# Optimization experiments

Hardware: AMD Instinct MI355X
Metric: run time of the kernel (lower is better)

The kernel has to match this reference:

```python
import jax, jax.numpy as jnp
import numpy as np

DIM = 512        # model dim
MOE_DIM = 256    # expert hidden dim
E = 64           # n_routed experts
G = 8            # n_routed_group
TOPK_G = 4       # n_topk_group
K = 8            # n_experts_per_tok
SCALE = 2.5      # routed_scale
CAP = 1024


def setup_inputs() -> dict:
    key = jax.random.key(0)
    ks = jax.random.split(key, 6)
    x = jax.random.normal(ks[0], (4, 512, DIM), jnp.float32)
    gate_w = jax.random.normal(ks[1], (E, DIM), jnp.float32) / np.sqrt(DIM).astype(np.float32)
    gate_b = jax.random.normal(ks[2], (E,), jnp.float32) * 0.01
    w1 = jax.random.normal(ks[3], (E, DIM, MOE_DIM), jnp.float32) / np.sqrt(DIM).astype(np.float32)
    w3 = jax.random.normal(ks[4], (E, DIM, MOE_DIM), jnp.float32) / np.sqrt(DIM).astype(np.float32)
    w2 = jax.random.normal(ks[5], (E, MOE_DIM, DIM), jnp.float32) / np.sqrt(MOE_DIM).astype(np.float32)
    return {"x": x, "gate_w": gate_w, "gate_b": gate_b, "w1": w1, "w3": w3, "w2": w2}


def _gate(x2, gate_w, gate_b):
    # x2: [T, DIM] -> (weights [T,K], indices [T,K])
    T = x2.shape[0]
    scores = jax.nn.sigmoid(x2 @ gate_w.T)                      # [T, E]
    s = (scores + gate_b).reshape(T, G, E // G)                  # grouped scores
    group_scores = jax.lax.top_k(s, 2)[0].sum(-1)                # [T, G] sum of top-2 per group
    top_groups = jax.lax.top_k(group_scores, TOPK_G)[1]          # [T, TOPK_G]
    gmask = jnp.zeros((T, G), bool).at[jnp.arange(T)[:, None], top_groups].set(True)
    s = jnp.where(gmask[..., None], s, -jnp.inf).reshape(T, E)
    idx = jax.lax.top_k(s, K)[1]                                 # [T, K]
    w = jnp.take_along_axis(scores, idx, axis=1)                 # original (pre-bias) scores
    w = w / w.sum(-1, keepdims=True) * SCALE
    return w, idx


def _moe_forward(x, gate_w, gate_b, w1, w3, w2):
    shape = x.shape
    x2 = x.reshape(-1, DIM)                                      # [T, DIM]
    T = x2.shape[0]
    w, idx = _gate(x2, gate_w, gate_b)
    flat_e = idx.reshape(-1)                                     # [T*K]
    # position of each (token, slot) within its expert's buffer, in order
    oh = (flat_e[:, None] == jnp.arange(E)[None, :]).astype(jnp.int32)  # [T*K, E]
    pos = (jnp.cumsum(oh, axis=0) * oh).sum(-1) - 1              # [T*K]
    x_rep = jnp.repeat(x2, K, axis=0)                            # [T*K, DIM]
    # dispatch into per-expert buffers [E, CAP, DIM]
    xb = jnp.zeros((E, CAP, DIM), x2.dtype).at[flat_e, pos].set(x_rep, mode='drop')
    h = jax.nn.silu(jnp.einsum('ecd,edm->ecm', xb, w1)) * jnp.einsum('ecd,edm->ecm', xb, w3)
    yb = jnp.einsum('ecm,emd->ecd', h, w2)                       # [E, CAP, DIM]
    # combine: gather back and weight
    y = yb.at[flat_e, pos].get(mode='fill', fill_value=0.0) * w.reshape(-1)[:, None]
    return y.reshape(T, K, DIM).sum(1).reshape(shape)


def reference(x, gate_w, gate_b, w1, w3, w2):
    return _moe_forward(x, gate_w, gate_b, w1, w3, w2)
```

## Files before the change

### kernel.cpp

```cpp
#include <hip/hip_runtime.h>

#define T_TOK 2048
#define DIM   512
#define MOE   256
#define NE    64
#define NG    8
#define TOPKG 4
#define TOPK  8
#define CAP   1024
#define MOE_SCALE 2.5f

typedef float f32x4 __attribute__((ext_vector_type(4)));
typedef short s16x8 __attribute__((ext_vector_type(8)));

__device__ __forceinline__ unsigned short f2bf(float f) {
    unsigned u = __builtin_bit_cast(unsigned, f);
    unsigned r = (u + 0x7fffu + ((u >> 16) & 1u)) >> 16;
    return (unsigned short)r;
}
__device__ __forceinline__ unsigned pk2(float lo, float hi) {
    return (unsigned)f2bf(lo) | ((unsigned)f2bf(hi) << 16);
}

__global__ __launch_bounds__(256) void gwt_k(const float* __restrict__ gw,
                                             float* __restrict__ gwT)
{
    int idx = blockIdx.x * 256 + threadIdx.x;
    int e = idx >> 9, k = idx & 511;
    gwT[(size_t)(k >> 2) * 256 + e * 4 + (k & 3)] = gw[idx];
}

__global__ __launch_bounds__(256) void gate_fused_k(const float* __restrict__ x,
                                                    const float* __restrict__ gwT,
                                                    const float* __restrict__ gb,
                                                    int* __restrict__ counts,
                                                    int* __restrict__ etok,
                                                    float* __restrict__ wt_of,
                                                    short* __restrict__ xb)
{
    __shared__ float xs[4][512];
    int w = threadIdx.x >> 6, lane = threadIdx.x & 63;
    int t = blockIdx.x * 4 + w;

    {
        const float4* xr = (const float4*)(x + (size_t)t * DIM);
        float4 v0 = xr[lane * 2], v1 = xr[lane * 2 + 1];
        *(float4*)&xs[w][lane * 8]     = v0;
        *(float4*)&xs[w][lane * 8 + 4] = v1;
        short o[8];
        o[0] = (short)f2bf(v0.x); o[1] = (short)f2bf(v0.y);
        o[2] = (short)f2bf(v0.z); o[3] = (short)f2bf(v0.w);
        o[4] = (short)f2bf(v1.x); o[5] = (short)f2bf(v1.y);
        o[6] = (short)f2bf(v1.z); o[7] = (short)f2bf(v1.w);
        *(s16x8*)(xb + (size_t)t * DIM + lane * 8) = *(const s16x8*)o;
    }
    __syncthreads();

    const float4* gt = (const float4*)gwT;
    float a0 = 0.f, a1 = 0.f, a2 = 0.f, a3 = 0.f;
#pragma unroll 4
    for (int k4 = 0; k4 < 128; k4 += 4) {
        float4 g0 = gt[(k4 + 0) * 64 + lane];
        float4 g1 = gt[(k4 + 1) * 64 + lane];
        float4 g2 = gt[(k4 + 2) * 64 + lane];
        float4 g3 = gt[(k4 + 3) * 64 + lane];
        float4 x0 = *(const float4*)&xs[w][(k4 + 0) * 4];
        float4 x1 = *(const float4*)&xs[w][(k4 + 1) * 4];
        float4 x2 = *(const float4*)&xs[w][(k4 + 2) * 4];
        float4 x3 = *(const float4*)&xs[w][(k4 + 3) * 4];
        a0 += g0.x * x0.x + g0.y * x0.y + g0.z * x0.z + g0.w * x0.w;
        a1 += g1.x * x1.x + g1.y * x1.y + g1.z * x1.z + g1.w * x1.w;
        a2 += g2.x * x2.x + g2.y * x2.y + g2.z * x2.z + g2.w * x2.w;
        a3 += g3.x * x3.x + g3.y * x3.y + g3.z * x3.z + g3.w * x3.w;
    }
    float acc = (a0 + a1) + (a2 + a3);
    float sc = 1.f / (1.f + __expf(-acc));
    float s  = sc + gb[lane];

    float m1 = s, m2 = -1e30f;
#pragma unroll
    for (int d = 1; d < 8; d <<= 1) {
        float o1 = __shfl_xor(m1, d);
        float o2 = __shfl_xor(m2, d);
        float n1 = fmaxf(m1, o1);
        float n2 = fmaxf(fminf(m1, o1), fmaxf(m2, o2));
        m1 = n1; m2 = n2;
    }
    float gv = m1 + m2;

    bool gkeep = false;
#pragma unroll
    for (int it = 0; it < TOPKG; ++it) {
        float m = gv;
#pragma unroll
        for (int d = 1; d < 64; d <<= 1) m = fmaxf(m, __shfl_xor(m, d));
        unsigned long long mask = __ballot(gv == m);
        int ldr = __ffsll(mask) - 1;
        if ((lane >> 3) == (ldr >> 3)) { gkeep = true; gv = -2e30f; }
    }
    float sv = gkeep ? s : -1e30f;

    float wsum = 0.f;
    int my_e = 0; float my_w = 0.f;
#pragma unroll
    for (int k = 0; k < TOPK; ++k) {
        float m = sv;
#pragma unroll
        for (int d = 1; d < 64; d <<= 1) m = fmaxf(m, __shfl_xor(m, d));
        unsigned long long mask = __ballot(sv == m);
        int l = __ffsll(mask) - 1;
        float wk = __shfl(sc, l);
        wsum += wk;
        if (lane == k) { my_e = l; my_w = wk; }
        if (lane == l) sv = -2e30f;
    }
    float scale = MOE_SCALE / wsum;
    if (lane < TOPK) {
        int p = atomicAdd(&counts[my_e], 1);
        int rid = t * TOPK + lane;
        bool ok = (p < CAP);
        if (ok) etok[my_e * CAP + p] = rid;
        wt_of[rid] = ok ? my_w * scale : 0.f;
    }
}

__global__ __launch_bounds__(64) void scan_k(const int* __restrict__ counts,
                                             int* __restrict__ tbase)
{
    int lane = threadIdx.x;
    int ne = min(counts[lane], CAP);
    int nt = (ne + 31) >> 5;
    int v = nt;
#pragma unroll
    for (int d = 1; d < 64; d <<= 1) {
        int o = __shfl_up(v, d);
        if (lane >= d) v += o;
    }
    tbase[lane] = v - nt;
}

__global__ __launch_bounds__(256, 3) void gemm1_k(const short* __restrict__ xb,
                                                  const float* __restrict__ w1,
                                                  const float* __restrict__ w3,
                                                  const int* __restrict__ counts,
                                                  const int* __restrict__ etok,
                                                  const int* __restrict__ tbase,
                                                  short* __restrict__ hgf)
{
    __shared__ short Bl[2][16][64][8];
    __shared__ short Ct[4][2][16][24];

    int e  = blockIdx.x & 63, cg = blockIdx.x >> 6;
    int n0 = cg * 16;
    int tid = threadIdx.x;
    int w = tid >> 6, lane = tid & 63;
    int q = lane >> 4, m16 = lane & 15;

    const float* W1e = w1 + (size_t)e * DIM * MOE + n0;
    const float* W3e = w3 + (size_t)e * DIM * MOE + n0;
#pragma unroll 4
    for (int it = 0; it < 8; ++it) {
        int idx = it * 256 + tid;
        int mat = idx >> 10;
        int rem = idx & 1023;
        int r2  = rem >> 2;
        int cq  = (rem & 3) * 4;
        int k   = r2 * 2;
        int kt = k >> 5, qf = (k >> 3) & 3, j0 = k & 7;
        const float* p = (mat ? W3e : W1e) + (size_t)k * MOE + cq;
        float4 lo = *(const float4*)p;
        float4 hi = *(const float4*)(p + MOE);
        unsigned* b = (unsigned*)&Bl[mat][kt][qf * 16 + cq][j0];
        b[0]  = pk2(lo.x, hi.x);
        b[4]  = pk2(lo.y, hi.y);
        b[8]  = pk2(lo.z, hi.z);
        b[12] = pk2(lo.w, hi.w);
    }
    __syncthreads();

    int ne = min(counts[e], CAP);
    int nt = (ne + 31) >> 5;
    int G0 = tbase[e];
    const int* el = etok + e * CAP;

    for (int T = w; T < nt; T += 4) {
        int row0 = T * 32 + m16, row1 = T * 32 + 16 + m16;
        int tok0 = el[row0 < ne ? row0 : ne - 1] >> 3;
        int tok1 = el[row1 < ne ? row1 : ne - 1] >> 3;
        const short* A0 = xb + (size_t)tok0 * DIM + q * 8;
        const short* A1 = xb + (size_t)tok1 * DIM + q * 8;

        f32x4 acc[2][2];
#pragma unroll
        for (int j = 0; j < 2; ++j)
#pragma unroll
            for (int m = 0; m < 2; ++m) acc[j][m] = (f32x4)0.f;

        s16x8 a0 = *(const s16x8*)(A0);
        s16x8 a1 = *(const s16x8*)(A1);
#pragma unroll
        for (int kt = 0; kt < 16; ++kt) {
            s16x8 a0n, a1n;
            if (kt < 15) {
                a0n = *(const s16x8*)(A0 + (kt + 1) * 32);
                a1n = *(const s16x8*)(A1 + (kt + 1) * 32);
            }
            s16x8 b1 = *(const s16x8*)&Bl[0][kt][lane][0];
            s16x8 b3 = *(const s16x8*)&Bl[1][kt][lane][0];
            acc[0][0] = __builtin_amdgcn_mfma_f32_16x16x32_bf16(a0, b1, acc[0][0], 0, 0, 0);
            acc[1][0] = __builtin_amdgcn_mfma_f32_16x16x32_bf16(a1, b1, acc[1][0], 0, 0, 0);
            acc[0][1] = __builtin_amdgcn_mfma_f32_16x16x32_bf16(a0, b3, acc[0][1], 0, 0, 0);
            acc[1][1] = __builtin_amdgcn_mfma_f32_16x16x32_bf16(a1, b3, acc[1][1], 0, 0, 0);
            a0 = a0n; a1 = a1n;
        }

#pragma unroll
        for (int sub = 0; sub < 2; ++sub)
#pragma unroll
            for (int r = 0; r < 4; ++r) {
                float g = acc[sub][0][r];
                float u = acc[sub][1][r];
                float hv = g / (1.f + __expf(-g)) * u;
                Ct[w][sub][q * 4 + r][m16] = (short)f2bf(hv);
            }
        int sub = q >> 1;
        s16x8 hv8 = *(const s16x8*)&Ct[w][sub][m16][(q & 1) * 8];
        size_t slot = ((size_t)(G0 + T) * 8 + (cg >> 1)) * 2 + sub;
        *(s16x8*)(hgf + slot * 512 + ((cg & 1) * 2 + (q & 1)) * 128 + m16 * 8) = hv8;
    }
}

__global__ __launch_bounds__(256, 3) void gemm2_k(const short* __restrict__ hgf,
                                                  const float* __restrict__ w2,
                                                  const int* __restrict__ counts,
                                                  const int* __restrict__ etok,
                                                  const int* __restrict__ tbase,
                                                  short* __restrict__ ybuf)
{
    __shared__ short Bl[2][8][64][8];

    int e  = blockIdx.x & 63, cg = blockIdx.x >> 6;
    int n0 = cg * 32;
    int tid = threadIdx.x;
    int w = tid >> 6, lane = tid & 63;
    int q = lane >> 4, m16 = lane & 15;

    const float* W2e = w2 + (size_t)e * MOE * DIM + n0;
#pragma unroll 4
    for (int it = 0; it < 4; ++it) {
        int idx = it * 256 + tid;
        int r2  = idx >> 3;
        int cq  = (idx & 7) * 4;
        int k   = r2 * 2;
        int kt2 = k >> 5, qf = (k >> 3) & 3, j0 = k & 7;
        int s = cq >> 4, c15 = cq & 15;
        const float* p = W2e + (size_t)k * DIM + cq;
        float4 lo = *(const float4*)p;
        float4 hi = *(const float4*)(p + DIM);
        unsigned* b = (unsigned*)&Bl[s][kt2][qf * 16 + c15][j0];
        b[0]  = pk2(lo.x, hi.x);
        b[4]  = pk2(lo.y, hi.y);
        b[8]  = pk2(lo.z, hi.z);
        b[12] = pk2(lo.w, hi.w);
    }
    __syncthreads();

    int ne = min(counts[e], CAP);
    int nt = (ne + 31) >> 5;
    int G0 = tbase[e];
    const int* el = etok + e * CAP;

    for (int T = w; T < nt; T += 4) {
        const short* A = hgf + (size_t)(G0 + T) * 8192 + lane * 8;

        f32x4 acc[2][2];
#pragma unroll
        for (int j = 0; j < 2; ++j)
#pragma unroll
            for (int m = 0; m < 2; ++m) acc[j][m] = (f32x4)0.f;

        s16x8 a0 = *(const s16x8*)(A);
        s16x8 a1 = *(const s16x8*)(A + 512);
#pragma unroll
        for (int kt = 0; kt < 8; ++kt) {
            s16x8 a0n, a1n;
            if (kt < 7) {
                a0n = *(const s16x8*)(A + (size_t)((kt + 1) * 2 + 0) * 512);
                a1n = *(const s16x8*)(A + (size_t)((kt + 1) * 2 + 1) * 512);
            }
            s16x8 b0 = *(const s16x8*)&Bl[0][kt][lane][0];
            s16x8 b1 = *(const s16x8*)&Bl[1][kt][lane][0];
            acc[0][0] = __builtin_amdgcn_mfma_f32_16x16x32_bf16(a0, b0, acc[0][0], 0, 0, 0);
            acc[1][0] = __builtin_amdgcn_mfma_f32_16x16x32_bf16(a1, b0, acc[1][0], 0, 0, 0);
            acc[0][1] = __builtin_amdgcn_mfma_f32_16x16x32_bf16(a0, b1, acc[0][1], 0, 0, 0);
            acc[1][1] = __builtin_amdgcn_mfma_f32_16x16x32_bf16(a1, b1, acc[1][1], 0, 0, 0);
            a0 = a0n; a1 = a1n;
        }

#pragma unroll
        for (int sub = 0; sub < 2; ++sub)
#pragma unroll
            for (int s = 0; s < 2; ++s)
#pragma unroll
                for (int r = 0; r < 4; ++r) {
                    int row = T * 32 + sub * 16 + q * 4 + r;
                    if (row < ne)
                        ybuf[(size_t)el[row] * DIM + n0 + s * 16 + m16] =
                            (short)f2bf(acc[sub][s][r]);
                }
    }
}

__global__ __launch_bounds__(256) void combine_k(const short* __restrict__ ybuf,
                                                 const float* __restrict__ wt_of,
                                                 float* __restrict__ out)
{
    int t = blockIdx.x;
    int tid = threadIdx.x;
    const int* yb = (const int*)ybuf;
    float sx = 0.f, sy = 0.f;
#pragma unroll
    for (int k = 0; k < TOPK; ++k) {
        float wk = wt_of[t * TOPK + k];
        int v = yb[(size_t)(t * TOPK + k) * (DIM / 2) + tid];
        float lo = __builtin_bit_cast(float, (unsigned)v << 16);
        float hi = __builtin_bit_cast(float, (unsigned)v & 0xffff0000u);
        sx += wk * lo;
        sy += wk * hi;
    }
    float2 o = {sx, sy};
    ((float2*)out)[(size_t)t * (DIM / 2) + tid] = o;
}

extern "C" void kernel_launch(void* const* d_in, const int* in_sizes, int n_in,
                              void* d_out, int out_size, void* d_ws, size_t ws_size,
                              hipStream_t stream)
{
    const float* x  = (const float*)d_in[0];
    const float* gw = (const float*)d_in[1];
    const float* gb = (const float*)d_in[2];
    const float* w1 = (const float*)d_in[3];
    const float* w3 = (const float*)d_in[4];
    const float* w2 = (const float*)d_in[5];

    char* ws = (char*)d_ws;
    short* xb    = (short*)(ws);
    short* hgf   = (short*)(ws + 2097152);
    short* ybuf  = (short*)(ws + 11534336);
    float* gwT   = (float*)(ws + 28311552);
    int*   etok  = (int*)  (ws + 28442624);
    float* wt_of = (float*)(ws + 28704768);
    int*   counts= (int*)  (ws + 28770304);
    int*   tbase = (int*)  (ws + 28770560);

    hipMemsetAsync(counts, 0, NE * 4, stream);

    gwt_k<<<128, 256, 0, stream>>>(gw, gwT);
    gate_fused_k<<<T_TOK / 4, 256, 0, stream>>>(x, gwT, gb, counts, etok, wt_of, xb);
    scan_k<<<1, 64, 0, stream>>>(counts, tbase);
    gemm1_k<<<NE * 16, 256, 0, stream>>>(xb, w1, w3, counts, etok, tbase, hgf);
    gemm2_k<<<NE * 16, 256, 0, stream>>>(hgf, w2, counts, etok, tbase, ybuf);
    combine_k<<<T_TOK, 256, 0, stream>>>(ybuf, wt_of, (float*)d_out);
}
```

Before: 248.8 us.

## Widen expert GEMM column tiles, deepen A prefetch, split gate dot over waves

Each expert GEMM block now covers twice as many output columns, using 32 for gemm1 and 64 for gemm2, with half as many blocks. This reuses each gathered A fragment across more MFMAs and halves how often activations are re-read per expert. A loads are prefetched four k-steps ahead, the next tile's token indices are prefetched, and weight loads use nontemporal hints. The gate kernel splits the K dimension across waves so each gwT load is shared by four tokens, then reduces the partial sums through shared memory. The trade-off is higher register and LDS use, with launch bounds lowered to two blocks, and fewer blocks to spread the load across CUs.

```diff
diff --git a/kernel.cpp b/kernel.cpp
--- a/kernel.cpp
+++ b/kernel.cpp
@@ -39,6 +39,7 @@
                                                     short* __restrict__ xb)
 {
     __shared__ float xs[4][512];
+    __shared__ float ps[4][4][64];
     int w = threadIdx.x >> 6, lane = threadIdx.x & 63;
     int t = blockIdx.x * 4 + w;
 
@@ -56,24 +57,26 @@
     }
     __syncthreads();
 
-    const float4* gt = (const float4*)gwT;
+    const f32x4* gt = (const f32x4*)gwT;
     float a0 = 0.f, a1 = 0.f, a2 = 0.f, a3 = 0.f;
-#pragma unroll 4
-    for (int k4 = 0; k4 < 128; k4 += 4) {
-        float4 g0 = gt[(k4 + 0) * 64 + lane];
-        float4 g1 = gt[(k4 + 1) * 64 + lane];
-        float4 g2 = gt[(k4 + 2) * 64 + lane];
-        float4 g3 = gt[(k4 + 3) * 64 + lane];
-        float4 x0 = *(const float4*)&xs[w][(k4 + 0) * 4];
-        float4 x1 = *(const float4*)&xs[w][(k4 + 1) * 4];
-        float4 x2 = *(const float4*)&xs[w][(k4 + 2) * 4];
-        float4 x3 = *(const float4*)&xs[w][(k4 + 3) * 4];
-        a0 += g0.x * x0.x + g0.y * x0.y + g0.z * x0.z + g0.w * x0.w;
-        a1 += g1.x * x1.x + g1.y * x1.y + g1.z * x1.z + g1.w * x1.w;
-        a2 += g2.x * x2.x + g2.y * x2.y + g2.z * x2.z + g2.w * x2.w;
-        a3 += g3.x * x3.x + g3.y * x3.y + g3.z * x3.z + g3.w * x3.w;
-    }
-    float acc = (a0 + a1) + (a2 + a3);
+    int kb = w * 32;
+#pragma unroll 8
+    for (int k4 = 0; k4 < 32; ++k4) {
+        f32x4 g  = gt[(size_t)(kb + k4) * 64 + lane];
+        f32x4 x0 = *(const f32x4*)&xs[0][(kb + k4) * 4];
+        f32x4 x1 = *(const f32x4*)&xs[1][(kb + k4) * 4];
+        f32x4 x2 = *(const f32x4*)&xs[2][(kb + k4) * 4];
+        f32x4 x3 = *(const f32x4*)&xs[3][(kb + k4) * 4];
+        a0 += g.x * x0.x + g.y * x0.y + g.z * x0.z + g.w * x0.w;
+        a1 += g.x * x1.x + g.y * x1.y + g.z * x1.z + g.w * x1.w;
+        a2 += g.x * x2.x + g.y * x2.y + g.z * x2.z + g.w * x2.w;
+        a3 += g.x * x3.x + g.y * x3.y + g.z * x3.z + g.w * x3.w;
+    }
+    ps[w][0][lane] = a0; ps[w][1][lane] = a1;
+    ps[w][2][lane] = a2; ps[w][3][lane] = a3;
+    __syncthreads();
+    float acc = ps[0][w][lane] + ps[1][w][lane] + ps[2][w][lane] + ps[3][w][lane];
+
     float sc = 1.f / (1.f + __expf(-acc));
     float s  = sc + gb[lane];
 
@@ -139,7 +142,7 @@
     tbase[lane] = v - nt;
 }
 
-__global__ __launch_bounds__(256, 3) void gemm1_k(const short* __restrict__ xb,
+__global__ __launch_bounds__(256, 2) void gemm1_k(const short* __restrict__ xb,
                                                   const float* __restrict__ w1,
                                                   const float* __restrict__ w3,
                                                   const int* __restrict__ counts,
@@ -147,11 +150,11 @@
                                                   const int* __restrict__ tbase,
                                                   short* __restrict__ hgf)
 {
-    __shared__ short Bl[2][16][64][8];
+    __shared__ short Bl[2][16][2][64][8];
     __shared__ short Ct[4][2][16][24];
 
     int e  = blockIdx.x & 63, cg = blockIdx.x >> 6;
-    int n0 = cg * 16;
+    int n0 = cg * 32;
     int tid = threadIdx.x;
     int w = tid >> 6, lane = tid & 63;
     int q = lane >> 4, m16 = lane & 15;
@@ -159,18 +162,19 @@
     const float* W1e = w1 + (size_t)e * DIM * MOE + n0;
     const float* W3e = w3 + (size_t)e * DIM * MOE + n0;
 #pragma unroll 4
-    for (int it = 0; it < 8; ++it) {
+    for (int it = 0; it < 16; ++it) {
         int idx = it * 256 + tid;
-        int mat = idx >> 10;
-        int rem = idx & 1023;
-        int r2  = rem >> 2;
-        int cq  = (rem & 3) * 4;
+        int mat = idx >> 11;
+        int rem = idx & 2047;
+        int r2  = rem >> 3;
+        int cq  = (rem & 7) * 4;
         int k   = r2 * 2;
         int kt = k >> 5, qf = (k >> 3) & 3, j0 = k & 7;
+        int cgrp = cq >> 4, c15 = cq & 15;
         const float* p = (mat ? W3e : W1e) + (size_t)k * MOE + cq;
-        float4 lo = *(const float4*)p;
-        float4 hi = *(const float4*)(p + MOE);
-        unsigned* b = (unsigned*)&Bl[mat][kt][qf * 16 + cq][j0];
+        f32x4 lo = __builtin_nontemporal_load((const f32x4*)p);
+        f32x4 hi = __builtin_nontemporal_load((const f32x4*)(p + MOE));
+        unsigned* b = (unsigned*)&Bl[mat][kt][cgrp][qf * 16 + c15][j0];
         b[0]  = pk2(lo.x, hi.x);
         b[4]  = pk2(lo.y, hi.y);
         b[8]  = pk2(lo.z, hi.z);
@@ -183,80 +187,103 @@
     int G0 = tbase[e];
     const int* el = etok + e * CAP;
 
+    int row0 = w * 32 + m16, row1 = row0 + 16;
+    int tr0 = 0, tr1 = 0;
+    if (w < nt) {
+        tr0 = el[row0 < ne ? row0 : ne - 1];
+        tr1 = el[row1 < ne ? row1 : ne - 1];
+    }
+
     for (int T = w; T < nt; T += 4) {
-        int row0 = T * 32 + m16, row1 = T * 32 + 16 + m16;
-        int tok0 = el[row0 < ne ? row0 : ne - 1] >> 3;
-        int tok1 = el[row1 < ne ? row1 : ne - 1] >> 3;
-        const short* A0 = xb + (size_t)tok0 * DIM + q * 8;
-        const short* A1 = xb + (size_t)tok1 * DIM + q * 8;
-
-        f32x4 acc[2][2];
-#pragma unroll
-        for (int j = 0; j < 2; ++j)
-#pragma unroll
-            for (int m = 0; m < 2; ++m) acc[j][m] = (f32x4)0.f;
-
-        s16x8 a0 = *(const s16x8*)(A0);
-        s16x8 a1 = *(const s16x8*)(A1);
+        const short* A0 = xb + (size_t)(tr0 >> 3) * DIM + q * 8;
+        const short* A1 = xb + (size_t)(tr1 >> 3) * DIM + q * 8;
+        if (T + 4 < nt) {
+            int nr0 = (T + 4) * 32 + m16, nr1 = nr0 + 16;
+            tr0 = el[nr0 < ne ? nr0 : ne - 1];
+            tr1 = el[nr1 < ne ? nr1 : ne - 1];
+        }
+
+        f32x4 acc[2][2][2];
+#pragma unroll
+        for (int i = 0; i < 2; ++i)
+#pragma unroll
+            for (int j = 0; j < 2; ++j)
+#pragma unroll
+                for (int c = 0; c < 2; ++c) acc[i][j][c] = (f32x4)0.f;
+
+        s16x8 pa0[4], pa1[4];
+#pragma unroll
+        for (int i = 0; i < 4; ++i) {
+            pa0[i] = *(const s16x8*)(A0 + i * 32);
+            pa1[i] = *(const s16x8*)(A1 + i * 32);
+        }
 #pragma unroll
         for (int kt = 0; kt < 16; ++kt) {
-            s16x8 a0n, a1n;
-            if (kt < 15) {
-                a0n = *(const s16x8*)(A0 + (kt + 1) * 32);
-                a1n = *(const s16x8*)(A1 + (kt + 1) * 32);
+            s16x8 a0 = pa0[kt & 3], a1 = pa1[kt & 3];
+            if (kt < 12) {
+                pa0[kt & 3] = *(const s16x8*)(A0 + (kt + 4) * 32);
+                pa1[kt & 3] = *(const s16x8*)(A1 + (kt + 4) * 32);
             }
-            s16x8 b1 = *(const s16x8*)&Bl[0][kt][lane][0];
-            s16x8 b3 = *(const s16x8*)&Bl[1][kt][lane][0];
-            acc[0][0] = __builtin_amdgcn_mfma_f32_16x16x32_bf16(a0, b1, acc[0][0], 0, 0, 0);
-            acc[1][0] = __builtin_amdgcn_mfma_f32_16x16x32_bf16(a1, b1, acc[1][0], 0, 0, 0);
-            acc[0][1] = __builtin_amdgcn_mfma_f32_16x16x32_bf16(a0, b3, acc[0][1], 0, 0, 0);
-            acc[1][1] = __builtin_amdgcn_mfma_f32_16x16x32_bf16(a1, b3, acc[1][1], 0, 0, 0);
-            a0 = a0n; a1 = a1n;
-        }
-
-#pragma unroll
-        for (int sub = 0; sub < 2; ++sub)
-#pragma unroll
-            for (int r = 0; r < 4; ++r) {
-                float g = acc[sub][0][r];
-                float u = acc[sub][1][r];
-                float hv = g / (1.f + __expf(-g)) * u;
-                Ct[w][sub][q * 4 + r][m16] = (short)f2bf(hv);
-            }
-        int sub = q >> 1;
-        s16x8 hv8 = *(const s16x8*)&Ct[w][sub][m16][(q & 1) * 8];
-        size_t slot = ((size_t)(G0 + T) * 8 + (cg >> 1)) * 2 + sub;
-        *(s16x8*)(hgf + slot * 512 + ((cg & 1) * 2 + (q & 1)) * 128 + m16 * 8) = hv8;
-    }
-}
-
-__global__ __launch_bounds__(256, 3) void gemm2_k(const short* __restrict__ hgf,
+            s16x8 b10 = *(const s16x8*)&Bl[0][kt][0][lane][0];
+            s16x8 b11 = *(const s16x8*)&Bl[0][kt][1][lane][0];
+            s16x8 b30 = *(const s16x8*)&Bl[1][kt][0][lane][0];
+            s16x8 b31 = *(const s16x8*)&Bl[1][kt][1][lane][0];
+            acc[0][0][0] = __builtin_amdgcn_mfma_f32_16x16x32_bf16(a0, b10, acc[0][0][0], 0, 0, 0);
+            acc[1][0][0] = __builtin_amdgcn_mfma_f32_16x16x32_bf16(a1, b10, acc[1][0][0], 0, 0, 0);
+            acc[0][0][1] = __builtin_amdgcn_mfma_f32_16x16x32_bf16(a0, b11, acc[0][0][1], 0, 0, 0);
+            acc[1][0][1] = __builtin_amdgcn_mfma_f32_16x16x32_bf16(a1, b11, acc[1][0][1], 0, 0, 0);
+            acc[0][1][0] = __builtin_amdgcn_mfma_f32_16x16x32_bf16(a0, b30, acc[0][1][0], 0, 0, 0);
+            acc[1][1][0] = __builtin_amdgcn_mfma_f32_16x16x32_bf16(a1, b30, acc[1][1][0], 0, 0, 0);
+            acc[0][1][1] = __builtin_amdgcn_mfma_f32_16x16x32_bf16(a0, b31, acc[0][1][1], 0, 0, 0);
+            acc[1][1][1] = __builtin_amdgcn_mfma_f32_16x16x32_bf16(a1, b31, acc[1][1][1], 0, 0, 0);
+        }
+
+#pragma unroll
+        for (int cgrp = 0; cgrp < 2; ++cgrp) {
+#pragma unroll
+            for (int sub = 0; sub < 2; ++sub)
+#pragma unroll
+                for (int r = 0; r < 4; ++r) {
+                    float g = acc[sub][0][cgrp][r];
+                    float u = acc[sub][1][cgrp][r];
+                    float hv = g / (1.f + __expf(-g)) * u;
+                    Ct[w][sub][q * 4 + r][m16] = (short)f2bf(hv);
+                }
+            int subr = q >> 1;
+            s16x8 hv8 = *(const s16x8*)&Ct[w][subr][m16][(q & 1) * 8];
+            size_t slot = ((size_t)(G0 + T) * 8 + cg) * 2 + subr;
+            *(s16x8*)(hgf + slot * 512 + (cgrp * 2 + (q & 1)) * 128 + m16 * 8) = hv8;
+        }
+    }
+}
+
+__global__ __launch_bounds__(256, 2) void gemm2_k(const short* __restrict__ hgf,
                                                   const float* __restrict__ w2,
                                                   const int* __restrict__ counts,
                                                   const int* __restrict__ etok,
                                                   const int* __restrict__ tbase,
                                                   short* __restrict__ ybuf)
 {
-    __shared__ short Bl[2][8][64][8];
+    __shared__ short Bl[4][8][64][8];
 
     int e  = blockIdx.x & 63, cg = blockIdx.x >> 6;
-    int n0 = cg * 32;
+    int n0 = cg * 64;
     int tid = threadIdx.x;
     int w = tid >> 6, lane = tid & 63;
     int q = lane >> 4, m16 = lane & 15;
 
     const float* W2e = w2 + (size_t)e * MOE * DIM + n0;
 #pragma unroll 4
-    for (int it = 0; it < 4; ++it) {
+    for (int it = 0; it < 8; ++it) {
         int idx = it * 256 + tid;
-        int r2  = idx >> 3;
-        int cq  = (idx & 7) * 4;
+        int r2  = idx >> 4;
+        int cq  = (idx & 15) * 4;
         int k   = r2 * 2;
         int kt2 = k >> 5, qf = (k >> 3) & 3, j0 = k & 7;
         int s = cq >> 4, c15 = cq & 15;
         const float* p = W2e + (size_t)k * DIM + cq;
-        float4 lo = *(const float4*)p;
-        float4 hi = *(const float4*)(p + DIM);
+        f32x4 lo = __builtin_nontemporal_load((const f32x4*)p);
+        f32x4 hi = __builtin_nontemporal_load((const f32x4*)(p + DIM));
         unsigned* b = (unsigned*)&Bl[s][kt2][qf * 16 + c15][j0];
         b[0]  = pk2(lo.x, hi.x);
         b[4]  = pk2(lo.y, hi.y);
@@ -273,39 +300,56 @@
     for (int T = w; T < nt; T += 4) {
         const short* A = hgf + (size_t)(G0 + T) * 8192 + lane * 8;
 
-        f32x4 acc[2][2];
-#pragma unroll
-        for (int j = 0; j < 2; ++j)
-#pragma unroll
-            for (int m = 0; m < 2; ++m) acc[j][m] = (f32x4)0.f;
-
-        s16x8 a0 = *(const s16x8*)(A);
-        s16x8 a1 = *(const s16x8*)(A + 512);
+        int erid[2][4];
+#pragma unroll
+        for (int sub = 0; sub < 2; ++sub)
+#pragma unroll
+            for (int r = 0; r < 4; ++r) {
+                int row = T * 32 + sub * 16 + q * 4 + r;
+                erid[sub][r] = row < ne ? el[row] : -1;
+            }
+
+        f32x4 acc[2][4];
+#pragma unroll
+        for (int i = 0; i < 2; ++i)
+#pragma unroll
+            for (int j = 0; j < 4; ++j) acc[i][j] = (f32x4)0.f;
+
+        s16x8 pa0[4], pa1[4];
+#pragma unroll
+        for (int i = 0; i < 4; ++i) {
+            pa0[i] = *(const s16x8*)(A + (i * 2 + 0) * 512);
+            pa1[i] = *(const s16x8*)(A + (i * 2 + 1) * 512);
+        }
 #pragma unroll
         for (int kt = 0; kt < 8; ++kt) {
-            s16x8 a0n, a1n;
-            if (kt < 7) {
-                a0n = *(const s16x8*)(A + (size_t)((kt + 1) * 2 + 0) * 512);
-                a1n = *(const s16x8*)(A + (size_t)((kt + 1) * 2 + 1) * 512);
+            s16x8 a0 = pa0[kt & 3], a1 = pa1[kt & 3];
+            if (kt < 4) {
+                pa0[kt & 3] = *(const s16x8*)(A + ((kt + 4) * 2 + 0) * 512);
+                pa1[kt & 3] = *(const s16x8*)(A + ((kt + 4) * 2 + 1) * 512);
             }
             s16x8 b0 = *(const s16x8*)&Bl[0][kt][lane][0];
             s16x8 b1 = *(const s16x8*)&Bl[1][kt][lane][0];
+            s16x8 b2 = *(const s16x8*)&Bl[2][kt][lane][0];
+            s16x8 b3 = *(const s16x8*)&Bl[3][kt][lane][0];
             acc[0][0] = __builtin_amdgcn_mfma_f32_16x16x32_bf16(a0, b0, acc[0][0], 0, 0, 0);
             acc[1][0] = __builtin_amdgcn_mfma_f32_16x16x32_bf16(a1, b0, acc[1][0], 0, 0, 0);
             acc[0][1] = __builtin_amdgcn_mfma_f32_16x16x32_bf16(a0, b1, acc[0][1], 0, 0, 0);
             acc[1][1] = __builtin_amdgcn_mfma_f32_16x16x32_bf16(a1, b1, acc[1][1], 0, 0, 0);
-            a0 = a0n; a1 = a1n;
+            acc[0][2] = __builtin_amdgcn_mfma_f32_16x16x32_bf16(a0, b2, acc[0][2], 0, 0, 0);
+            acc[1][2] = __builtin_amdgcn_mfma_f32_16x16x32_bf16(a1, b2, acc[1][2], 0, 0, 0);
+            acc[0][3] = __builtin_amdgcn_mfma_f32_16x16x32_bf16(a0, b3, acc[0][3], 0, 0, 0);
+            acc[1][3] = __builtin_amdgcn_mfma_f32_16x16x32_bf16(a1, b3, acc[1][3], 0, 0, 0);
         }
 
 #pragma unroll
         for (int sub = 0; sub < 2; ++sub)
 #pragma unroll
-            for (int s = 0; s < 2; ++s)
+            for (int s = 0; s < 4; ++s)
 #pragma unroll
                 for (int r = 0; r < 4; ++r) {
-                    int row = T * 32 + sub * 16 + q * 4 + r;
-                    if (row < ne)
-                        ybuf[(size_t)el[row] * DIM + n0 + s * 16 + m16] =
+                    if (erid[sub][r] >= 0)
+                        ybuf[(size_t)erid[sub][r] * DIM + n0 + s * 16 + m16] =
                             (short)f2bf(acc[sub][s][r]);
                 }
     }
@@ -358,7 +402,7 @@
     gwt_k<<<128, 256, 0, stream>>>(gw, gwT);
     gate_fused_k<<<T_TOK / 4, 256, 0, stream>>>(x, gwT, gb, counts, etok, wt_of, xb);
     scan_k<<<1, 64, 0, stream>>>(counts, tbase);
-    gemm1_k<<<NE * 16, 256, 0, stream>>>(xb, w1, w3, counts, etok, tbase, hgf);
-    gemm2_k<<<NE * 16, 256, 0, stream>>>(hgf, w2, counts, etok, tbase, ybuf);
+    gemm1_k<<<NE * 8, 256, 0, stream>>>(xb, w1, w3, counts, etok, tbase, hgf);
+    gemm2_k<<<NE * 8, 256, 0, stream>>>(hgf, w2, counts, etok, tbase, ybuf);
     combine_k<<<T_TOK, 256, 0, stream>>>(ybuf, wt_of, (float*)d_out);
 }
```

After: 240.6 us. -3.3%, faster.
